# Kernel tuning notes

Hardware: AMD Instinct MI355X
Metric: run time of the kernel (lower is better)

## Reference

```python
import jax, jax.numpy as jnp
import numpy as np

B, N, H = 32, 2048, 128
L4H = 4 * H  # concatenated (c0,h0,c1,h1) embedding dim


def _lstm_cell(x, c, h, Wx, Wh, b):
    g = x @ Wx + h @ Wh + b                      # [B,N,4H]
    i, f, gg, o = jnp.split(g, 4, axis=-1)
    c_new = jax.nn.sigmoid(f) * c + jax.nn.sigmoid(i) * jnp.tanh(gg)
    h_new = jax.nn.sigmoid(o) * jnp.tanh(c_new)
    return c_new, h_new


def setup_inputs() -> dict:
    key = jax.random.key(0)
    ks = jax.random.split(key, 20)
    s = 0.05
    inp = {
        'node_embeddings': jax.random.normal(ks[0], (B, N, H), jnp.float32),
        'c0': jax.random.normal(ks[1], (B, N, H), jnp.float32),
        'h0': jax.random.normal(ks[2], (B, N, H), jnp.float32),
        'c1': jax.random.normal(ks[3], (B, N, H), jnp.float32),
        'h1': jax.random.normal(ks[4], (B, N, H), jnp.float32),
        'instruction_pointer': jax.random.uniform(ks[5], (B, N), jnp.float32),
        'Wx0': s * jax.random.normal(ks[6], (H, 4 * H), jnp.float32),
        'Wh0': s * jax.random.normal(ks[7], (H, 4 * H), jnp.float32),
        'b0': jnp.zeros((4 * H,), jnp.float32),
        'Wx1': s * jax.random.normal(ks[8], (H, 4 * H), jnp.float32),
        'Wh1': s * jax.random.normal(ks[9], (H, 4 * H), jnp.float32),
        'b1': jnp.zeros((4 * H,), jnp.float32),
        'raise_W': s * jax.random.normal(ks[10], (L4H, 2), jnp.float32),
        'raise_b': jnp.zeros((2,), jnp.float32),
        'branch_W': s * jax.random.normal(ks[11], (L4H, 2), jnp.float32),
        'branch_b': jnp.zeros((2,), jnp.float32),
        'true_indexes': jax.random.randint(ks[12], (B, N), 0, N, jnp.int32),
        'false_indexes': jax.random.randint(ks[13], (B, N), 0, N, jnp.int32),
        'raise_indexes': jax.random.randint(ks[14], (B, N), 0, N, jnp.int32),
        'exit_node_indexes': jax.random.randint(ks[15], (B,), 0, N, jnp.int32),
        'raise_node_indexes': jax.random.randint(ks[16], (B,), 0, N, jnp.int32),
        'current_step': jnp.zeros((B,), jnp.int32),
        'step_limits': jax.random.randint(ks[17], (B,), 1, 100, jnp.int32),
    }
    return inp


def reference(node_embeddings, c0, h0, c1, h1, instruction_pointer,
              Wx0, Wh0, b0, Wx1, Wh1, b1, raise_W, raise_b, branch_W, branch_b,
              true_indexes, false_indexes, raise_indexes,
              exit_node_indexes, raise_node_indexes, current_step, step_limits):
    num_nodes = node_embeddings.shape[1]

    # --- execute: stacked 2-layer LSTM per node (vectorized over B,N) ---
    c0n, h0n = _lstm_cell(node_embeddings, c0, h0, Wx0, Wh0, b0)
    c1n, h1n = _lstm_cell(h0n, c1, h1, Wx1, Wh1, b1)
    old = (c0, h0, c1, h1)
    contrib = (c0n, h0n, c1n, h1n)

    # --- mask exit and raise nodes: keep old hidden state there ---
    node_ids = jnp.arange(num_nodes)[None, :]                  # [1,N]
    m_exit = node_ids == exit_node_indexes[:, None]            # [B,N]
    m_raise = node_ids == raise_node_indexes[:, None]          # [B,N]
    m_keep = (m_exit | m_raise)[..., None]                     # raise_in_ipagnn=True
    contrib = tuple(jnp.where(m_keep, o, c) for o, c in zip(old, contrib))

    # --- raise / branch decisions ---
    emb = jnp.concatenate(contrib, axis=-1)                    # [B,N,4H]
    raise_dec = jax.nn.softmax(emb @ raise_W + raise_b, axis=-1)
    raise_dec = jnp.where(m_exit[..., None], jnp.array([0.0, 1.0], raise_dec.dtype), raise_dec)
    branch_dec = jax.nn.softmax(emb @ branch_W + branch_b, axis=-1)

    p_raise = raise_dec[..., 0]
    p_noraise = raise_dec[..., 1]
    p_true = p_noraise * branch_dec[..., 0]
    p_false = p_noraise * branch_dec[..., 1]

    seg = jax.vmap(lambda d, i: jax.ops.segment_sum(d, i, num_segments=num_nodes))

    # --- instruction pointer update (scatter-add over soft edges) ---
    ip = instruction_pointer
    ip_new = (seg(p_raise * ip, raise_indexes)
              + seg(p_true * ip, true_indexes)
              + seg(p_false * ip, false_indexes))               # [B,N]

    # --- hidden-state aggregation, weighted by instruction pointer ---
    denom = (ip_new + 1e-7)[..., None]                          # [B,N,1]
    wr = (p_raise * ip)[..., None]
    wt = (p_true * ip)[..., None]
    wf = (p_false * ip)[..., None]
    agg = tuple((seg(hc * wr, raise_indexes)
                 + seg(hc * wt, true_indexes)
                 + seg(hc * wf, false_indexes)) / denom
                for hc in contrib)

    # --- keep old state if example already hit its step limit ---
    live = (current_step < step_limits)                         # [B]
    ip_fin = jnp.where(live[:, None], ip_new, ip)
    hid_fin = tuple(jnp.where(live[:, None, None], a, o) for a, o in zip(agg, old))

    # pack carry: (c0,h0,c1,h1) embedding + instruction pointer -> [B,N,4H+1]
    return jnp.concatenate(list(hid_fin) + [ip_fin[..., None]], axis=-1)
```

## Files before the change

kernel.cpp:

```cpp
#include <hip/hip_runtime.h>
#include <hip/hip_bf16.h>

constexpr int Bc  = 32;
constexpr int Nc  = 2048;
constexpr int Hc  = 128;
constexpr int H4c = 512;
constexpr int BNc = Bc * Nc;

typedef __attribute__((ext_vector_type(8))) short short8;
typedef __attribute__((ext_vector_type(4))) float f32x4;

__device__ __forceinline__ float sigf(float x)  { return 1.f / (1.f + __expf(-x)); }
__device__ __forceinline__ float tanh_(float x) { return 1.f - 2.f / (__expf(2.f * x) + 1.f); }

__device__ __forceinline__ unsigned short bfu(float f) {
    union { float f; unsigned u; } a; a.f = f;
    unsigned u = a.u;
    return (unsigned short)((u + 0x7FFFu + ((u >> 16) & 1u)) >> 16);
}
__device__ __forceinline__ float bf2f(unsigned short u) {
    union { unsigned u; float f; } a; a.u = ((unsigned)u) << 16;
    return a.f;
}
__device__ __forceinline__ unsigned cvtpk(float lo, float hi) {
    unsigned r;
    asm("v_cvt_pk_bf16_f32 %0, %1, %2" : "=v"(r) : "v"(lo), "v"(hi));
    return r;
}

__device__ __forceinline__ int a_off(int buf, int row, int byte) {
    return buf * 5120 + row * 80 + byte;
}
__device__ __forceinline__ int cs_off(int row, int unit) {
    return row * 512 + ((unit ^ (row & 7)) << 4);
}

__global__ __launch_bounds__(256) void prep_kernel(
    const float* __restrict__ Wx0, const float* __restrict__ Wh0,
    const float* __restrict__ Wx1, const float* __restrict__ Wh1,
    unsigned short* __restrict__ W0F, unsigned short* __restrict__ W1F,
    int* __restrict__ head)
{
    int idx = blockIdx.x * 256 + threadIdx.x;
    int4 m1 = { -1, -1, -1, -1 };
    ((int4*)head)[idx] = m1;

    int ct = idx >> 9, ks = (idx >> 6) & 7, lane = idx & 63;
    int col = ct * 16 + (lane & 15);
    unsigned short* p0 = W0F + (size_t)idx * 8;
    unsigned short* p1 = W1F + (size_t)idx * 8;
    #pragma unroll
    for (int e = 0; e < 8; ++e) {
        int k = ks * 32 + (lane >> 4) * 8 + e;
        float v0 = (k < 128) ? Wx0[k * 512 + col] : Wh0[(k - 128) * 512 + col];
        float v1 = (k < 128) ? Wx1[k * 512 + col] : Wh1[(k - 128) * 512 + col];
        p0[e] = bfu(v0);
        p1[e] = bfu(v1);
    }
}

__global__ __launch_bounds__(512, 4) void gemm0_kernel(
    const float* __restrict__ x_in,  const float* __restrict__ c0_in,
    const float* __restrict__ h0_in,
    const unsigned short* __restrict__ W0F, const float* __restrict__ b0,
    const int* __restrict__ exit_i, const int* __restrict__ raise_i,
    unsigned short* __restrict__ contrib)
{
    __shared__ __align__(16) char Ab[10240];
    __shared__ __align__(16) char Cs[32768];

    const int t    = threadIdx.x;
    const int w    = t >> 6, l = t & 63, lr = l & 15, lg = l >> 4;
    const int row0 = blockIdx.x * 64;
    const int bidx = row0 >> 11;
    const int eb   = exit_i[bidx];
    const int rbn  = raise_i[bidx];
    const int j    = w * 16 + lr;

    const int srow = t >> 3, sfq = t & 7;
#define STAGE0(c, bi)                                                          \
    {                                                                          \
        const float* sp = ((c) < 4 ? x_in : h0_in)                             \
            + (size_t)(row0 + srow) * Hc + ((c) & 3) * 32 + sfq * 4;           \
        float4 v = *(const float4*)sp;                                         \
        uint2 b2 = { cvtpk(v.x, v.y), cvtpk(v.z, v.w) };                       \
        *(uint2*)(Ab + a_off(bi, srow, sfq * 8)) = b2;                         \
    }

    f32x4 acc[4][4];
    #pragma unroll
    for (int g = 0; g < 4; ++g) {
        float bv = b0[g * 128 + j];
        f32x4 vv = {bv, bv, bv, bv};
        #pragma unroll
        for (int mt = 0; mt < 4; ++mt) acc[mt][g] = vv;
    }

    STAGE0(0, 0);
    short8 bn[4];
    #pragma unroll
    for (int g = 0; g < 4; ++g)
        bn[g] = *(const short8*)(W0F + ((size_t)((g * 8 + w) * 8) * 64 + l) * 8);
    #pragma unroll
    for (int c = 0; c < 8; ++c) {
        __syncthreads();
        short8 bc[4];
        #pragma unroll
        for (int g = 0; g < 4; ++g) bc[g] = bn[g];
        if (c < 7) {
            STAGE0(c + 1, (c + 1) & 1);
            #pragma unroll
            for (int g = 0; g < 4; ++g)
                bn[g] = *(const short8*)(W0F + ((size_t)((g * 8 + w) * 8 + c + 1) * 64 + l) * 8);
        }
        short8 a[4];
        #pragma unroll
        for (int mt = 0; mt < 4; ++mt)
            a[mt] = *(const short8*)(Ab + a_off(c & 1, mt * 16 + lr, lg * 16));
        #pragma unroll
        for (int mt = 0; mt < 4; ++mt)
            #pragma unroll
            for (int g = 0; g < 4; ++g)
                acc[mt][g] = __builtin_amdgcn_mfma_f32_16x16x32_bf16(
                    a[mt], bc[g], acc[mt][g], 0, 0, 0);
    }

    #pragma unroll
    for (int mt = 0; mt < 4; ++mt) {
        #pragma unroll
        for (int rr = 0; rr < 4; ++rr) {
            const int row  = mt * 16 + lg * 4 + rr;
            const int grow = row0 + row;
            const int n    = grow & (Nc - 1);
            float cold = c0_in[(size_t)grow * Hc + j];
            float ig = sigf(acc[mt][0][rr]);
            float fg = sigf(acc[mt][1][rr]);
            float gv = tanh_(acc[mt][2][rr]);
            float og = sigf(acc[mt][3][rr]);
            float cn = fg * cold + ig * gv;
            float hn = og * tanh_(cn);
            const bool keep = (n == eb) || (n == rbn);
            float cw = keep ? cold : cn;
            float hw = hn;
            if (keep) hw = h0_in[(size_t)grow * Hc + j];
            *(unsigned short*)(Cs + cs_off(row, j >> 3) + (j & 7) * 2)        = bfu(cw);
            *(unsigned short*)(Cs + cs_off(row, 16 + (j >> 3)) + (j & 7) * 2) = bfu(hw);
        }
    }
    __syncthreads();
    #pragma unroll
    for (int i = 0; i < 4; ++i) {
        const int idx = i * 512 + t;
        const int r = idx >> 5, u = idx & 31;
        short8 v = *(const short8*)(Cs + cs_off(r, u));
        *(short8*)(contrib + (size_t)(row0 + r) * H4c + u * 8) = v;
    }
#undef STAGE0
}

__global__ __launch_bounds__(512, 4) void gemm1_kernel(
    const unsigned short* __restrict__ contrib_r, const float* __restrict__ c1_in,
    const float* __restrict__ h1_in,
    const unsigned short* __restrict__ W1F, const float* __restrict__ b1,
    const float* __restrict__ rW, const float* __restrict__ rbv,
    const float* __restrict__ bW, const float* __restrict__ bbv,
    const float* __restrict__ ip_in,
    const int* __restrict__ exit_i, const int* __restrict__ raise_i,
    unsigned short* __restrict__ contrib, float* __restrict__ w_all)
{
    __shared__ __align__(16) char Ab[10240];
    __shared__ __align__(16) char Cs[32768];

    const int t    = threadIdx.x;
    const int w    = t >> 6, l = t & 63, lr = l & 15, lg = l >> 4;
    const int row0 = blockIdx.x * 64;
    const int bidx = row0 >> 11;
    const int eb   = exit_i[bidx];
    const int rbn  = raise_i[bidx];
    const int j    = w * 16 + lr;

    const int srow = t >> 3, sfq = t & 7;
#define STAGE1(c, bi)                                                          \
    {                                                                          \
        if ((c) < 4) {                                                         \
            ushort4 v = *(const ushort4*)(contrib_r                            \
                + (size_t)(row0 + srow) * H4c + 128 + ((c) & 3) * 32 + sfq * 4); \
            *(ushort4*)(Ab + a_off(bi, srow, sfq * 8)) = v;                    \
        } else {                                                               \
            const float* sp = h1_in + (size_t)(row0 + srow) * Hc               \
                + ((c) & 3) * 32 + sfq * 4;                                    \
            float4 v = *(const float4*)sp;                                     \
            uint2 b2 = { cvtpk(v.x, v.y), cvtpk(v.z, v.w) };                   \
            *(uint2*)(Ab + a_off(bi, srow, sfq * 8)) = b2;                     \
        }                                                                      \
    }

    f32x4 acc[4][4];
    #pragma unroll
    for (int g = 0; g < 4; ++g) {
        float bv = b1[g * 128 + j];
        f32x4 vv = {bv, bv, bv, bv};
        #pragma unroll
        for (int mt = 0; mt < 4; ++mt) acc[mt][g] = vv;
    }

    STAGE1(0, 0);
    short8 bn[4];
    #pragma unroll
    for (int g = 0; g < 4; ++g)
        bn[g] = *(const short8*)(W1F + ((size_t)((g * 8 + w) * 8) * 64 + l) * 8);
    #pragma unroll
    for (int c = 0; c < 8; ++c) {
        __syncthreads();
        short8 bc[4];
        #pragma unroll
        for (int g = 0; g < 4; ++g) bc[g] = bn[g];
        if (c < 7) {
            STAGE1(c + 1, (c + 1) & 1);
            #pragma unroll
            for (int g = 0; g < 4; ++g)
                bn[g] = *(const short8*)(W1F + ((size_t)((g * 8 + w) * 8 + c + 1) * 64 + l) * 8);
        }
        short8 a[4];
        #pragma unroll
        for (int mt = 0; mt < 4; ++mt)
            a[mt] = *(const short8*)(Ab + a_off(c & 1, mt * 16 + lr, lg * 16));
        #pragma unroll
        for (int mt = 0; mt < 4; ++mt)
            #pragma unroll
            for (int g = 0; g < 4; ++g)
                acc[mt][g] = __builtin_amdgcn_mfma_f32_16x16x32_bf16(
                    a[mt], bc[g], acc[mt][g], 0, 0, 0);
    }

    #pragma unroll
    for (int mt = 0; mt < 4; ++mt) {
        #pragma unroll
        for (int rr = 0; rr < 4; ++rr) {
            const int row  = mt * 16 + lg * 4 + rr;
            const int grow = row0 + row;
            const int n    = grow & (Nc - 1);
            float cold = c1_in[(size_t)grow * Hc + j];
            float ig = sigf(acc[mt][0][rr]);
            float fg = sigf(acc[mt][1][rr]);
            float gv = tanh_(acc[mt][2][rr]);
            float og = sigf(acc[mt][3][rr]);
            float cn = fg * cold + ig * gv;
            float hn = og * tanh_(cn);
            const bool keep = (n == eb) || (n == rbn);
            float cw = keep ? cold : cn;
            float hw = hn;
            if (keep) hw = h1_in[(size_t)grow * Hc + j];
            *(unsigned short*)(Cs + cs_off(row, j >> 3) + (j & 7) * 2)        = bfu(cw);
            *(unsigned short*)(Cs + cs_off(row, 16 + (j >> 3)) + (j & 7) * 2) = bfu(hw);
        }
    }
    __syncthreads();
    float* dw = (float*)Ab;
    if (t < 256) {
        ((float4*)dw)[t]       = ((const float4*)rW)[t];
        ((float4*)dw)[256 + t] = ((const float4*)bW)[t];
    }
    __syncthreads();
    #pragma unroll
    for (int i = 0; i < 4; ++i) {
        const int idx = i * 512 + t;
        const int r = idx >> 5, u = idx & 31;
        short8 v = *(const short8*)(Cs + cs_off(r, u));
        *(short8*)(contrib + (size_t)(row0 + r) * H4c + 256 + u * 8) = v;
    }

    {
        const int r8 = l >> 3, s = l & 7;
        const int row  = w * 8 + r8;
        const int grow = row0 + row;
        float pr0 = 0.f, pr1 = 0.f, pb0 = 0.f, pb1 = 0.f;
        #pragma unroll
        for (int cu = 0; cu < 8; ++cu) {
            short8 ev;
            if (s < 4)
                ev = *(const short8*)(contrib_r + (size_t)grow * H4c + s * 64 + cu * 8);
            else
                ev = *(const short8*)(Cs + cs_off(row, (s - 4) * 8 + cu));
            const int col0 = s * 64 + cu * 8;
            const float4* rp = (const float4*)(dw + col0 * 2);
            const float4* bp = (const float4*)(dw + 1024 + col0 * 2);
            #pragma unroll
            for (int q = 0; q < 4; ++q) {
                float4 rv = rp[q], bv = bp[q];
                float e0 = bf2f((unsigned short)ev[q * 2]);
                float e1 = bf2f((unsigned short)ev[q * 2 + 1]);
                pr0 += e0 * rv.x + e1 * rv.z;
                pr1 += e0 * rv.y + e1 * rv.w;
                pb0 += e0 * bv.x + e1 * bv.z;
                pb1 += e0 * bv.y + e1 * bv.w;
            }
        }
        #pragma unroll
        for (int m = 1; m < 8; m <<= 1) {
            pr0 += __shfl_xor(pr0, m);
            pr1 += __shfl_xor(pr1, m);
            pb0 += __shfl_xor(pb0, m);
            pb1 += __shfl_xor(pb1, m);
        }
        if (s == 0) {
            const int n = grow & (Nc - 1);
            float r0v = pr0 + rbv[0], r1v = pr1 + rbv[1];
            float m  = fmaxf(r0v, r1v);
            float z0 = __expf(r0v - m), z1 = __expf(r1v - m);
            float inv = 1.f / (z0 + z1);
            float praise = z0 * inv, pno = z1 * inv;
            if (n == eb) { praise = 0.f; pno = 1.f; }
            float q0 = pb0 + bbv[0], q1 = pb1 + bbv[1];
            float mm = fmaxf(q0, q1);
            float y0 = __expf(q0 - mm), y1 = __expf(q1 - mm);
            float binv = 1.f / (y0 + y1);
            float ipv = ip_in[grow];
            w_all[grow]            = praise * ipv;
            w_all[BNc + grow]      = pno * y0 * binv * ipv;
            w_all[2 * BNc + grow]  = pno * y1 * binv * ipv;
        }
    }
#undef STAGE1
}

__global__ __launch_bounds__(256) void build_kernel(
    const int* __restrict__ t_idx, const int* __restrict__ f_idx,
    const int* __restrict__ r_idx, int* __restrict__ head, int* __restrict__ nxt)
{
    const int row  = blockIdx.x * 256 + threadIdx.x;
    const int base = (row >> 11) << 11;
    const int e0 = row * 4;
    int o;
    o = atomicExch(&head[base + r_idx[row]], e0);     nxt[e0]     = o;
    o = atomicExch(&head[base + t_idx[row]], e0 + 1); nxt[e0 + 1] = o;
    o = atomicExch(&head[base + f_idx[row]], e0 + 2); nxt[e0 + 2] = o;
}

__global__ __launch_bounds__(256) void gather_kernel(
    const unsigned short* __restrict__ contrib, const float* __restrict__ w_all,
    const int* __restrict__ head, const int* __restrict__ nxt,
    const float* __restrict__ c0_in, const float* __restrict__ h0_in,
    const float* __restrict__ c1_in, const float* __restrict__ h1_in,
    const float* __restrict__ ip_in,
    const int* __restrict__ cstep, const int* __restrict__ slim,
    float* __restrict__ out)
{
    const int gtid = blockIdx.x * 256 + threadIdx.x;
    const int wid  = gtid >> 6;
    const int l    = gtid & 63;
    const int bidx = wid >> 11;

    float ax[4] = {0.f, 0.f, 0.f, 0.f};
    float ay[4] = {0.f, 0.f, 0.f, 0.f};
    float ipsum = 0.f;

    int e = head[wid];
    while (e >= 0) {
        const int src = e >> 2;
        const float w = w_all[(e & 3) * BNc + src];
        const unsigned* crow = (const unsigned*)(contrib + (size_t)src * 512);
        #pragma unroll
        for (int q = 0; q < 4; ++q) {
            unsigned pv = crow[q * 64 + l];
            ax[q] += w * bf2f((unsigned short)(pv & 0xFFFFu));
            ay[q] += w * bf2f((unsigned short)(pv >> 16));
        }
        ipsum += w;
        e = nxt[e];
    }

    const bool live = cstep[bidx] < slim[bidx];
    float* orow = out + (size_t)wid * 513;
    if (live) {
        const float inv = 1.f / (ipsum + 1e-7f);
        #pragma unroll
        for (int q = 0; q < 4; ++q) {
            const int idx0 = q * 128 + 2 * l;
            orow[idx0]     = ax[q] * inv;
            orow[idx0 + 1] = ay[q] * inv;
        }
        if (l == 0) orow[512] = ipsum;
    } else {
        #pragma unroll
        for (int q = 0; q < 4; ++q) {
            const float* p = q == 0 ? c0_in : q == 1 ? h0_in
                           : q == 2 ? c1_in : h1_in;
            float2 v = *(const float2*)(p + (size_t)wid * Hc + 2 * l);
            const int idx0 = q * 128 + 2 * l;
            orow[idx0]     = v.x;
            orow[idx0 + 1] = v.y;
        }
        if (l == 0) orow[512] = ip_in[wid];
    }
}

extern "C" void kernel_launch(void* const* d_in, const int* in_sizes, int n_in,
                              void* d_out, int out_size, void* d_ws, size_t ws_size,
                              hipStream_t stream) {
    const float* x     = (const float*)d_in[0];
    const float* c0    = (const float*)d_in[1];
    const float* h0    = (const float*)d_in[2];
    const float* c1    = (const float*)d_in[3];
    const float* h1    = (const float*)d_in[4];
    const float* ip    = (const float*)d_in[5];
    const float* Wx0   = (const float*)d_in[6];
    const float* Wh0   = (const float*)d_in[7];
    const float* b0    = (const float*)d_in[8];
    const float* Wx1   = (const float*)d_in[9];
    const float* Wh1   = (const float*)d_in[10];
    const float* b1    = (const float*)d_in[11];
    const float* rW    = (const float*)d_in[12];
    const float* rb    = (const float*)d_in[13];
    const float* bW    = (const float*)d_in[14];
    const float* bb    = (const float*)d_in[15];
    const int* t_idx   = (const int*)d_in[16];
    const int* f_idx   = (const int*)d_in[17];
    const int* r_idx   = (const int*)d_in[18];
    const int* exit_i  = (const int*)d_in[19];
    const int* raise_i = (const int*)d_in[20];
    const int* cstep   = (const int*)d_in[21];
    const int* slim    = (const int*)d_in[22];
    float* out = (float*)d_out;

    unsigned short* contrib = (unsigned short*)d_ws;
    unsigned short* W0F = contrib + (size_t)BNc * 512;
    unsigned short* W1F = W0F + 512 * 256;
    float* w_all = (float*)(W1F + 512 * 256);
    int*   head  = (int*)(w_all + 3 * (size_t)BNc);
    int*   nxt   = head + BNc;

    prep_kernel<<<64, 256, 0, stream>>>(Wx0, Wh0, Wx1, Wh1, W0F, W1F, head);
    build_kernel<<<BNc / 256, 256, 0, stream>>>(t_idx, f_idx, r_idx, head, nxt);
    gemm0_kernel<<<BNc / 64, 512, 0, stream>>>(x, c0, h0, W0F, b0,
                                               exit_i, raise_i, contrib);
    gemm1_kernel<<<BNc / 64, 512, 0, stream>>>(contrib, c1, h1, W1F, b1,
                                               rW, rb, bW, bb, ip,
                                               exit_i, raise_i, contrib, w_all);
    gather_kernel<<<BNc / 4, 256, 0, stream>>>(contrib, w_all, head, nxt,
                                               c0, h0, c1, h1, ip, cstep, slim, out);
}
```

Measured before the change: 197.9 us.

## Compute layer-0 half of raise/branch projections in gemm0 from shared memory

Moves the raise/branch logit dot products over the layer-0 (c0,h0) half of the embedding into gemm0, reading the freshly computed bf16 values from shared memory instead of having gemm1 re-read them from global contrib. gemm0 writes a per-row float4 of partial sums, which gemm1 adds to its own layer-1 half. The weight staging to shared memory is moved before the epilogue so one __syncthreads can be dropped. In exchange there is an extra small global buffer write and read, and gemm0 carries more epilogue work.

```diff
diff --git a/kernel.cpp b/kernel.cpp
--- a/kernel.cpp
+++ b/kernel.cpp
@@ -63,8 +63,9 @@
     const float* __restrict__ x_in,  const float* __restrict__ c0_in,
     const float* __restrict__ h0_in,
     const unsigned short* __restrict__ W0F, const float* __restrict__ b0,
+    const float* __restrict__ rW, const float* __restrict__ bW,
     const int* __restrict__ exit_i, const int* __restrict__ raise_i,
-    unsigned short* __restrict__ contrib)
+    unsigned short* __restrict__ contrib, float4* __restrict__ w_part)
 {
     __shared__ __align__(16) char Ab[10240];
     __shared__ __align__(16) char Cs[32768];
@@ -124,6 +125,10 @@
                 acc[mt][g] = __builtin_amdgcn_mfma_f32_16x16x32_bf16(
                     a[mt], bc[g], acc[mt][g], 0, 0, 0);
     }
+
+    float* dwA = (float*)Ab;
+    if (t < 128)      ((float4*)dwA)[t]       = ((const float4*)rW)[t];
+    else if (t < 256) ((float4*)dwA)[t]       = ((const float4*)bW)[t - 128];
 
     #pragma unroll
     for (int mt = 0; mt < 4; ++mt) {
@@ -155,6 +160,43 @@
         short8 v = *(const short8*)(Cs + cs_off(r, u));
         *(short8*)(contrib + (size_t)(row0 + r) * H4c + u * 8) = v;
     }
+
+    {
+        const int r8 = l >> 3, s = l & 7;
+        const int row  = w * 8 + r8;
+        const int grow = row0 + row;
+        float pr0 = 0.f, pr1 = 0.f, pb0 = 0.f, pb1 = 0.f;
+        if (s < 4) {
+            #pragma unroll
+            for (int cu = 0; cu < 8; ++cu) {
+                short8 ev = *(const short8*)(Cs + cs_off(row, s * 8 + cu));
+                const int col0 = s * 64 + cu * 8;
+                const float4* rp = (const float4*)(dwA + col0 * 2);
+                const float4* bp = (const float4*)(dwA + 512 + col0 * 2);
+                #pragma unroll
+                for (int q = 0; q < 4; ++q) {
+                    float4 rv = rp[q], bv = bp[q];
+                    float e0 = bf2f((unsigned short)ev[q * 2]);
+                    float e1 = bf2f((unsigned short)ev[q * 2 + 1]);
+                    pr0 += e0 * rv.x + e1 * rv.z;
+                    pr1 += e0 * rv.y + e1 * rv.w;
+                    pb0 += e0 * bv.x + e1 * bv.z;
+                    pb1 += e0 * bv.y + e1 * bv.w;
+                }
+            }
+        }
+        #pragma unroll
+        for (int m = 1; m < 8; m <<= 1) {
+            pr0 += __shfl_xor(pr0, m);
+            pr1 += __shfl_xor(pr1, m);
+            pb0 += __shfl_xor(pb0, m);
+            pb1 += __shfl_xor(pb1, m);
+        }
+        if (s == 0) {
+            float4 wp = { pr0, pr1, pb0, pb1 };
+            w_part[grow] = wp;
+        }
+    }
 #undef STAGE0
 }
 
@@ -164,7 +206,7 @@
     const unsigned short* __restrict__ W1F, const float* __restrict__ b1,
     const float* __restrict__ rW, const float* __restrict__ rbv,
     const float* __restrict__ bW, const float* __restrict__ bbv,
-    const float* __restrict__ ip_in,
+    const float* __restrict__ ip_in, const float4* __restrict__ w_part,
     const int* __restrict__ exit_i, const int* __restrict__ raise_i,
     unsigned short* __restrict__ contrib, float* __restrict__ w_all)
 {
@@ -232,6 +274,10 @@
                 acc[mt][g] = __builtin_amdgcn_mfma_f32_16x16x32_bf16(
                     a[mt], bc[g], acc[mt][g], 0, 0, 0);
     }
+
+    float* dw = (float*)Ab;
+    if (t < 128)      ((float4*)dw)[t] = ((const float4*)(rW + 512))[t];
+    else if (t < 256) ((float4*)dw)[t] = ((const float4*)(bW + 512))[t - 128];
 
     #pragma unroll
     for (int mt = 0; mt < 4; ++mt) {
@@ -256,12 +302,6 @@
         }
     }
     __syncthreads();
-    float* dw = (float*)Ab;
-    if (t < 256) {
-        ((float4*)dw)[t]       = ((const float4*)rW)[t];
-        ((float4*)dw)[256 + t] = ((const float4*)bW)[t];
-    }
-    __syncthreads();
     #pragma unroll
     for (int i = 0; i < 4; ++i) {
         const int idx = i * 512 + t;
@@ -275,25 +315,23 @@
         const int row  = w * 8 + r8;
         const int grow = row0 + row;
         float pr0 = 0.f, pr1 = 0.f, pb0 = 0.f, pb1 = 0.f;
-        #pragma unroll
-        for (int cu = 0; cu < 8; ++cu) {
-            short8 ev;
-            if (s < 4)
-                ev = *(const short8*)(contrib_r + (size_t)grow * H4c + s * 64 + cu * 8);
-            else
-                ev = *(const short8*)(Cs + cs_off(row, (s - 4) * 8 + cu));
-            const int col0 = s * 64 + cu * 8;
-            const float4* rp = (const float4*)(dw + col0 * 2);
-            const float4* bp = (const float4*)(dw + 1024 + col0 * 2);
-            #pragma unroll
-            for (int q = 0; q < 4; ++q) {
-                float4 rv = rp[q], bv = bp[q];
-                float e0 = bf2f((unsigned short)ev[q * 2]);
-                float e1 = bf2f((unsigned short)ev[q * 2 + 1]);
-                pr0 += e0 * rv.x + e1 * rv.z;
-                pr1 += e0 * rv.y + e1 * rv.w;
-                pb0 += e0 * bv.x + e1 * bv.z;
-                pb1 += e0 * bv.y + e1 * bv.w;
+        if (s >= 4) {
+            #pragma unroll
+            for (int cu = 0; cu < 8; ++cu) {
+                short8 ev = *(const short8*)(Cs + cs_off(row, (s - 4) * 8 + cu));
+                const int lcol = (s - 4) * 64 + cu * 8;
+                const float4* rp = (const float4*)(dw + lcol * 2);
+                const float4* bp = (const float4*)(dw + 512 + lcol * 2);
+                #pragma unroll
+                for (int q = 0; q < 4; ++q) {
+                    float4 rv = rp[q], bv = bp[q];
+                    float e0 = bf2f((unsigned short)ev[q * 2]);
+                    float e1 = bf2f((unsigned short)ev[q * 2 + 1]);
+                    pr0 += e0 * rv.x + e1 * rv.z;
+                    pr1 += e0 * rv.y + e1 * rv.w;
+                    pb0 += e0 * bv.x + e1 * bv.z;
+                    pb1 += e0 * bv.y + e1 * bv.w;
+                }
             }
         }
         #pragma unroll
@@ -304,6 +342,8 @@
             pb1 += __shfl_xor(pb1, m);
         }
         if (s == 0) {
+            float4 wp = w_part[grow];
+            pr0 += wp.x; pr1 += wp.y; pb0 += wp.z; pb1 += wp.w;
             const int n = grow & (Nc - 1);
             float r0v = pr0 + rbv[0], r1v = pr1 + rbv[1];
             float m  = fmaxf(r0v, r1v);
@@ -429,13 +469,14 @@
     float* w_all = (float*)(W1F + 512 * 256);
     int*   head  = (int*)(w_all + 3 * (size_t)BNc);
     int*   nxt   = head + BNc;
+    float4* w_part = (float4*)(nxt + 4 * (size_t)BNc);
 
     prep_kernel<<<64, 256, 0, stream>>>(Wx0, Wh0, Wx1, Wh1, W0F, W1F, head);
     build_kernel<<<BNc / 256, 256, 0, stream>>>(t_idx, f_idx, r_idx, head, nxt);
-    gemm0_kernel<<<BNc / 64, 512, 0, stream>>>(x, c0, h0, W0F, b0,
-                                               exit_i, raise_i, contrib);
+    gemm0_kernel<<<BNc / 64, 512, 0, stream>>>(x, c0, h0, W0F, b0, rW, bW,
+                                               exit_i, raise_i, contrib, w_part);
     gemm1_kernel<<<BNc / 64, 512, 0, stream>>>(contrib, c1, h1, W1F, b1,
-                                               rW, rb, bW, bb, ip,
+                                               rW, rb, bW, bb, ip, w_part,
                                                exit_i, raise_i, contrib, w_all);
     gather_kernel<<<BNc / 4, 256, 0, stream>>>(contrib, w_all, head, nxt,
                                                c0, h0, c1, h1, ip, cstep, slim, out);
```

Measured after the change: 214.8 us. +8.5%, slower.
